# Performance work log

Hardware: AMD Instinct MI355X
Metric: run time of the kernel (lower is better)

## Reference

```python
import jax, jax.numpy as jnp
import numpy as np

CUM_P = 0.9  # cumulative_p
MIN_KEEP = 1  # min_tokens_to_keep (<=1 -> branch is a no-op, as in torch default)


def setup_inputs() -> dict:
    key = jax.random.key(0)
    k1, k2 = jax.random.split(key, 2)
    B, D, V = 64, 2048, 50257
    x = jax.random.normal(k1, (B, D), dtype=jnp.float32)
    W = jax.random.normal(k2, (D, V), dtype=jnp.float32) * (1.0 / np.sqrt(D))
    b = jnp.zeros((V,), dtype=jnp.float32)
    return {"x": x, "W": W, "b": b}


def _nucleus_probs(x, W, b):
    # proj + softmax -> probs over vocab  [B, V]
    probs = jax.nn.softmax(x @ W + b, axis=-1)
    # descending sort over vocab
    sorted_idx = jnp.argsort(-probs, axis=-1)                      # [B, V]
    sorted_p = jnp.take_along_axis(probs, sorted_idx, axis=-1)    # [B, V]
    cum = jnp.cumsum(sorted_p, axis=-1)
    remove_sorted = cum > CUM_P
    # shift right by one so the token that crosses the threshold is kept
    remove_sorted = jnp.concatenate(
        [jnp.zeros_like(remove_sorted[..., :1]), remove_sorted[..., :-1]], axis=-1
    )
    # scatter mask back to original vocab order
    rows = jnp.arange(probs.shape[0])[:, None]                     # [B, 1]
    remove = jnp.zeros_like(remove_sorted).at[rows, sorted_idx].set(remove_sorted)
    kept = jnp.where(remove, 0.0, probs)
    # renormalize exactly as torch: p * 1/(sum + 1e-6)
    return kept * (1.0 / (kept.sum(axis=-1, keepdims=True) + 1e-6))


def reference(x, W, b):
    p = _nucleus_probs(x, W, b)                                    # [B, V]
    # Categorical(probs).sample(); zeros -> log = -inf (never sampled)
    return jax.random.categorical(jax.random.key(42), jnp.log(p), axis=-1)
```

## Files before the change

### kernel.cpp

```cpp
#include <hip/hip_runtime.h>
#include <hip/hip_bf16.h>
#include <stdint.h>

#define BB 64
#define DD 2048
#define VV 50257
#define VP 50260
#define NQ 12565
#define RB 13
#define QPB 967
#define NB 4096
#define MAXC 2048
#define QS 8
#define QCH 6283
#define SK 4

typedef __attribute__((ext_vector_type(8))) short short8;
typedef __attribute__((ext_vector_type(4))) float f32x4;
typedef float f32x4u __attribute__((vector_size(16), aligned(4)));

struct U2 { unsigned x, y; };

__device__ __forceinline__ unsigned rotl32(unsigned v, int r) {
  return (v << r) | (v >> (32 - r));
}

__device__ __forceinline__ U2 threefry2x32(unsigned k0, unsigned k1,
                                           unsigned x0, unsigned x1) {
  unsigned k2 = k0 ^ k1 ^ 0x1BD11BDAu;
  x0 += k0; x1 += k1;
#define TF_R4(r1, r2, r3, r4)                         \
  x0 += x1; x1 = rotl32(x1, r1); x1 ^= x0;            \
  x0 += x1; x1 = rotl32(x1, r2); x1 ^= x0;            \
  x0 += x1; x1 = rotl32(x1, r3); x1 ^= x0;            \
  x0 += x1; x1 = rotl32(x1, r4); x1 ^= x0;
  TF_R4(13, 15, 26, 6)   x0 += k1; x1 += k2 + 1u;
  TF_R4(17, 29, 16, 24)  x0 += k2; x1 += k0 + 2u;
  TF_R4(13, 15, 26, 6)   x0 += k0; x1 += k1 + 3u;
  TF_R4(17, 29, 16, 24)  x0 += k1; x1 += k2 + 4u;
  TF_R4(13, 15, 26, 6)   x0 += k2; x1 += k0 + 5u;
#undef TF_R4
  U2 r; r.x = x0; r.y = x1; return r;
}

__device__ __forceinline__ unsigned jax_random_bits(unsigned e) {
  U2 r = threefry2x32(0u, 42u, 0u, e);
  return r.x ^ r.y;
}

__device__ __forceinline__ unsigned mono_key(float zi) {
  unsigned bb = __float_as_uint(zi);
  return bb ^ ((bb >> 31) ? 0xFFFFFFFFu : 0x80000000u);
}
__device__ __forceinline__ float mono_key_inv(unsigned k) {
  return __uint_as_float((k >> 31) ? (k ^ 0x80000000u) : ~k);
}

__device__ __forceinline__ unsigned short f2bf_hw(float f) {
  __hip_bfloat16 b = __float2bfloat16(f);
  unsigned short u;
  __builtin_memcpy(&u, &b, 2);
  return u;
}
__device__ __forceinline__ float bf2f(unsigned short h) {
  return __uint_as_float(((unsigned)h) << 16);
}

__global__ __launch_bounds__(256) void pack_x_kernel(
    const float* __restrict__ x, unsigned short* __restrict__ xh,
    unsigned short* __restrict__ xl, unsigned* __restrict__ rowmax) {
  if (blockIdx.x == 0 && threadIdx.x < BB) rowmax[threadIdx.x] = 0u;
  int i = blockIdx.x * 256 + threadIdx.x;
  if (i >= 64 * 256) return;
  int b = i >> 8;
  int c = i & 255;
  const float* xp = x + b * 2048 + c * 8;
  short8 hv, lv;
#pragma unroll
  for (int j = 0; j < 8; ++j) {
    float f = xp[j];
    unsigned short h = f2bf_hw(f);
    hv[j] = (short)h;
    lv[j] = (short)f2bf_hw(f - bf2f(h));
  }
  size_t p = ((size_t)c * 64 + b) * 8;
  *(short8*)(xh + p) = hv;
  *(short8*)(xl + p) = lv;
}

__global__ __launch_bounds__(256, 1) void gemm_mfma_kernel(
    const unsigned short* __restrict__ xh, const unsigned short* __restrict__ xl,
    const float* __restrict__ W, float* __restrict__ partial) {
  const int wave = threadIdx.x >> 6;
  const int lane = threadIdx.x & 63;
  const int lo = lane & 15, hi = lane >> 4;
  const int v0w = blockIdx.x * 256 + wave * 64;
  const int vC = v0w + 4 * lo;
  const int ks0 = blockIdx.y * 16;
  const bool edge = (v0w + 64 > VV);

  f32x4 a00 = {0,0,0,0}, a01 = {0,0,0,0}, a02 = {0,0,0,0}, a03 = {0,0,0,0};
  f32x4 a10 = {0,0,0,0}, a11 = {0,0,0,0}, a12 = {0,0,0,0}, a13 = {0,0,0,0};
  f32x4 a20 = {0,0,0,0}, a21 = {0,0,0,0}, a22 = {0,0,0,0}, a23 = {0,0,0,0};
  f32x4 a30 = {0,0,0,0}, a31 = {0,0,0,0}, a32 = {0,0,0,0}, a33 = {0,0,0,0};

  for (int kss = 0; kss < 16; ++kss) {
    const int ks = ks0 + kss;
    const float* wb = W + (size_t)(ks * 32 + hi * 8) * VV;
    f32x4u wq[8];
    if (!edge) {
#pragma unroll
      for (int j = 0; j < 8; ++j)
        wq[j] = *(const f32x4u*)(wb + (size_t)j * VV + vC);
    } else {
#pragma unroll
      for (int j = 0; j < 8; ++j) {
#pragma unroll
        for (int c = 0; c < 4; ++c) {
          int col = vC + c; if (col > VV - 1) col = VV - 1;
          wq[j][c] = wb[(size_t)j * VV + col];
        }
      }
    }
    short8 bh0, bh1, bh2, bh3, bl0, bl1, bl2, bl3;
#pragma unroll
    for (int j = 0; j < 8; ++j) {
      unsigned short h;
      h = f2bf_hw(wq[j][0]); bh0[j] = (short)h; bl0[j] = (short)f2bf_hw(wq[j][0] - bf2f(h));
      h = f2bf_hw(wq[j][1]); bh1[j] = (short)h; bl1[j] = (short)f2bf_hw(wq[j][1] - bf2f(h));
      h = f2bf_hw(wq[j][2]); bh2[j] = (short)h; bl2[j] = (short)f2bf_hw(wq[j][2] - bf2f(h));
      h = f2bf_hw(wq[j][3]); bh3[j] = (short)h; bl3[j] = (short)f2bf_hw(wq[j][3] - bf2f(h));
    }
    const int chunk = ks * 4 + hi;
#define DO_RT(RT, A0, A1, A2, A3)                                           \
    {                                                                       \
      size_t p = ((size_t)chunk * 64 + (RT) * 16 + lo) * 8;                 \
      short8 ah = *(const short8*)(xh + p);                                 \
      short8 al = *(const short8*)(xl + p);                                 \
      A0 = __builtin_amdgcn_mfma_f32_16x16x32_bf16(ah, bh0, A0, 0, 0, 0);   \
      A0 = __builtin_amdgcn_mfma_f32_16x16x32_bf16(al, bh0, A0, 0, 0, 0);   \
      A0 = __builtin_amdgcn_mfma_f32_16x16x32_bf16(ah, bl0, A0, 0, 0, 0);   \
      A1 = __builtin_amdgcn_mfma_f32_16x16x32_bf16(ah, bh1, A1, 0, 0, 0);   \
      A1 = __builtin_amdgcn_mfma_f32_16x16x32_bf16(al, bh1, A1, 0, 0, 0);   \
      A1 = __builtin_amdgcn_mfma_f32_16x16x32_bf16(ah, bl1, A1, 0, 0, 0);   \
      A2 = __builtin_amdgcn_mfma_f32_16x16x32_bf16(ah, bh2, A2, 0, 0, 0);   \
      A2 = __builtin_amdgcn_mfma_f32_16x16x32_bf16(al, bh2, A2, 0, 0, 0);   \
      A2 = __builtin_amdgcn_mfma_f32_16x16x32_bf16(ah, bl2, A2, 0, 0, 0);   \
      A3 = __builtin_amdgcn_mfma_f32_16x16x32_bf16(ah, bh3, A3, 0, 0, 0);   \
      A3 = __builtin_amdgcn_mfma_f32_16x16x32_bf16(al, bh3, A3, 0, 0, 0);   \
      A3 = __builtin_amdgcn_mfma_f32_16x16x32_bf16(ah, bl3, A3, 0, 0, 0);   \
    }
    DO_RT(0, a00, a10, a20, a30)
    DO_RT(1, a01, a11, a21, a31)
    DO_RT(2, a02, a12, a22, a32)
    DO_RT(3, a03, a13, a23, a33)
#undef DO_RT
  }

  float* pp = partial + (size_t)blockIdx.y * BB * VP;
#define ST_RT(RT, A0, A1, A2, A3)                                           \
  {                                                                         \
    _Pragma("unroll")                                                       \
    for (int r = 0; r < 4; ++r) {                                           \
      int row = (RT) * 16 + hi * 4 + r;                                     \
      float4 o; o.x = A0[r]; o.y = A1[r]; o.z = A2[r]; o.w = A3[r];         \
      if (!edge) {                                                          \
        *(float4*)(pp + (size_t)row * VP + vC) = o;                         \
      } else {                                                              \
        if (vC + 0 < VV) pp[(size_t)row * VP + vC + 0] = o.x;               \
        if (vC + 1 < VV) pp[(size_t)row * VP + vC + 1] = o.y;               \
        if (vC + 2 < VV) pp[(size_t)row * VP + vC + 2] = o.z;               \
        if (vC + 3 < VV) pp[(size_t)row * VP + vC + 3] = o.w;               \
      }                                                                     \
    }                                                                       \
  }
  ST_RT(0, a00, a10, a20, a30)
  ST_RT(1, a01, a11, a21, a31)
  ST_RT(2, a02, a12, a22, a32)
  ST_RT(3, a03, a13, a23, a33)
#undef ST_RT
}

__global__ __launch_bounds__(256) void reduce_bias_kernel(
    const float* __restrict__ partial, const float* __restrict__ bias,
    float* __restrict__ logits, unsigned* __restrict__ rowmax) {
  __shared__ float smax[256];
  const int b = blockIdx.y;
  const int q0 = blockIdx.x * QPB;
  const int q1 = (q0 + QPB < NQ) ? q0 + QPB : NQ;
  float mx = -3.4e38f;
  for (int q = q0 + threadIdx.x; q < q1; q += 256) {
    if (q < NQ - 1) {
      int v = q * 4;
      float4 acc = *(const float4*)(bias + v);
#pragma unroll
      for (int s = 0; s < SK; ++s) {
        float4 p = *(const float4*)(partial + ((size_t)s * BB + b) * VP + v);
        acc.x += p.x; acc.y += p.y; acc.z += p.z; acc.w += p.w;
      }
      *(float4*)(logits + (size_t)b * VP + v) = acc;
      mx = fmaxf(mx, fmaxf(fmaxf(acc.x, acc.y), fmaxf(acc.z, acc.w)));
    } else {
      int v = VV - 1;
      float acc = bias[v];
#pragma unroll
      for (int s = 0; s < SK; ++s)
        acc += partial[((size_t)s * BB + b) * VP + v];
      logits[(size_t)b * VP + v] = acc;
      mx = fmaxf(mx, acc);
    }
  }
  smax[threadIdx.x] = mx; __syncthreads();
  for (int s = 128; s > 0; s >>= 1) {
    if (threadIdx.x < s) smax[threadIdx.x] = fmaxf(smax[threadIdx.x], smax[threadIdx.x + s]);
    __syncthreads();
  }
  if (threadIdx.x == 0) atomicMax(rowmax + b, mono_key(smax[0]));
}

__global__ __launch_bounds__(1024) void nucleus_tstar_kernel(
    const float* __restrict__ logits, const unsigned* __restrict__ rowmax,
    unsigned* __restrict__ tstar_out, unsigned long long* __restrict__ pack) {
  __shared__ double sd[1024];
  __shared__ unsigned su[1024];
  __shared__ double bins[NB];
  __shared__ int cidx[MAXC];
  __shared__ unsigned ckey[MAXC];
  __shared__ double cw[MAXC];
  __shared__ int ccount;
  __shared__ int sh_chunk;
  __shared__ int sh_bstar;
  __shared__ double sh_sabove;

  const int row = blockIdx.x;
  const int tid = threadIdx.x;
  const float* z = logits + (size_t)row * VP;
  const float m = mono_key_inv(rowmax[row]);

  for (int i = tid; i < NB; i += 1024) bins[i] = 0.0;
  if (tid == 0) { ccount = 0; sh_chunk = -1; sh_bstar = -1; }
  __syncthreads();

  for (int i = tid; i < VV; i += 1024) {
    float zi = z[i];
    int bin = (int)((m - zi) * 256.0f);
    bin = (bin < 0) ? 0 : ((bin > NB - 1) ? NB - 1 : bin);
    atomicAdd(&bins[bin], (double)expf(zi - m));
  }
  __syncthreads();

  {
    double c = bins[4 * tid] + bins[4 * tid + 1] + bins[4 * tid + 2] + bins[4 * tid + 3];
    sd[tid] = c; __syncthreads();
    for (int off = 1; off < 1024; off <<= 1) {
      double vv = (tid >= off) ? sd[tid - off] : 0.0;
      __syncthreads();
      sd[tid] += vv;
      __syncthreads();
    }
  }
  const double Z = sd[1023];
  const double C = (double)0.9f * Z;

  if (sd[tid] > C && (tid == 0 || sd[tid - 1] <= C)) sh_chunk = tid;
  __syncthreads();
  if (tid == 0) {
    int tc = sh_chunk;
    if (tc >= 0) {
      double run = (tc > 0) ? sd[tc - 1] : 0.0;
      for (int k = 0; k < 4; ++k) {
        double bw = bins[4 * tc + k];
        if (run + bw > C) { sh_bstar = 4 * tc + k; sh_sabove = run; break; }
        run += bw;
      }
    }
  }
  __syncthreads();
  const int bstar = sh_bstar;
  unsigned tkey = 0u;

  if (bstar >= 0) {
    const double Sab = sh_sabove;
    for (int i = tid; i < VV; i += 1024) {
      float zi = z[i];
      int bin = (int)((m - zi) * 256.0f);
      bin = (bin < 0) ? 0 : ((bin > NB - 1) ? NB - 1 : bin);
      if (bin == bstar) {
        int slot = atomicAdd(&ccount, 1);
        if (slot < MAXC) {
          ckey[slot] = mono_key(zi);
          cidx[slot] = i;
          cw[slot] = (double)expf(zi - m);
        }
      }
    }
    __syncthreads();
    int n = ccount; if (n > MAXC) n = MAXC;
    unsigned mk = 0xFFFFFFFFu;
    for (int i = tid; i < n; i += 1024) {
      unsigned ki = ckey[i]; int ii = cidx[i];
      double T = Sab;
      for (int j = 0; j < n; ++j) {
        unsigned kj = ckey[j];
        if (kj > ki || (kj == ki && cidx[j] < ii)) T += cw[j];
      }
      if (T <= C) mk = (ki < mk) ? ki : mk;
    }
    su[tid] = mk; __syncthreads();
    for (int s = 512; s > 0; s >>= 1) {
      if (tid < s) su[tid] = min(su[tid], su[tid + s]);
      __syncthreads();
    }
    tkey = su[0];
  }
  if (tid == 0) { tstar_out[row] = tkey; pack[row] = 0ull; }
}

__global__ __launch_bounds__(1024) void gumbel_kernel(
    const float* __restrict__ logits, const unsigned* __restrict__ tstar_arr,
    unsigned long long* __restrict__ pack) {
  __shared__ float sf[1024];
  __shared__ int si[1024];
  const int row = blockIdx.x >> 3;
  const int q = blockIdx.x & 7;
  const int tid = threadIdx.x;
  const unsigned tstar = tstar_arr[row];
  const float* z = logits + (size_t)row * VP;
  const int i0 = q * QCH;
  const int i1 = (i0 + QCH < VV) ? (i0 + QCH) : VV;

  float best = -3.4e38f; int bidx = 0x7FFFFFFF;
  for (int i = i0 + tid; i < i1; i += 1024) {
    float zi = z[i];
    if (mono_key(zi) < tstar) continue;
    unsigned e = (unsigned)row * (unsigned)VV + (unsigned)i;
    unsigned bits = jax_random_bits(e);
    float f = __uint_as_float((bits >> 9) | 0x3F800000u) - 1.0f;
    float u = fmaxf(1.17549435082228750797e-38f, f);
    float g = -logf(-logf(u));
    float sc = zi + g;
    if (sc > best) { best = sc; bidx = i; }
  }
  sf[tid] = best; si[tid] = bidx; __syncthreads();
  for (int s = 512; s > 0; s >>= 1) {
    if (tid < s) {
      float ob = sf[tid + s]; int oi = si[tid + s];
      if (ob > sf[tid] || (ob == sf[tid] && oi < si[tid])) {
        sf[tid] = ob; si[tid] = oi;
      }
    }
    __syncthreads();
  }
  if (tid == 0 && si[0] != 0x7FFFFFFF) {
    unsigned long long p = ((unsigned long long)mono_key(sf[0]) << 32) |
                           (unsigned long long)(0xFFFFFFFFu - (unsigned)si[0]);
    atomicMax(pack + row, p);
  }
}

__global__ __launch_bounds__(64) void unpack_kernel(
    const unsigned long long* __restrict__ pack, int* __restrict__ out) {
  int r = threadIdx.x;
  if (r < BB) out[r] = (int)(0xFFFFFFFFu - (unsigned)(pack[r] & 0xFFFFFFFFull));
}

extern "C" void kernel_launch(void* const* d_in, const int* in_sizes, int n_in,
                              void* d_out, int out_size, void* d_ws, size_t ws_size,
                              hipStream_t stream) {
  const float* x = (const float*)d_in[0];
  const float* W = (const float*)d_in[1];
  const float* bias = (const float*)d_in[2];
  int* out = (int*)d_out;
  char* ws = (char*)d_ws;

  unsigned short* xh = (unsigned short*)ws;
  unsigned short* xl = (unsigned short*)(ws + 262144);
  float* logits = (float*)(ws + 524288);
  float* partial = (float*)(ws + 13390848);
  unsigned* tstar = (unsigned*)(ws + 64857088);
  unsigned long long* pack = (unsigned long long*)(ws + 64857344);
  unsigned* rowmax = (unsigned*)(ws + 64857856);

  pack_x_kernel<<<64, 256, 0, stream>>>(x, xh, xl, rowmax);
  const int cblocks = (VV + 255) / 256;
  dim3 g(cblocks, SK);
  gemm_mfma_kernel<<<g, 256, 0, stream>>>(xh, xl, W, partial);
  dim3 gr(RB, BB);
  reduce_bias_kernel<<<gr, 256, 0, stream>>>(partial, bias, logits, rowmax);
  nucleus_tstar_kernel<<<BB, 1024, 0, stream>>>(logits, rowmax, tstar, pack);
  gumbel_kernel<<<BB * QS, 1024, 0, stream>>>(logits, tstar, pack);
  unpack_kernel<<<1, 64, 0, stream>>>(pack, out);
}
```

Before: 184.8 us.

## Build histogram in reduce kernel with fixed bin origin, split nucleus into stages

```diff
diff --git a/kernel.cpp b/kernel.cpp
--- a/kernel.cpp
+++ b/kernel.cpp
@@ -9,7 +9,7 @@
 #define NQ 12565
 #define RB 13
 #define QPB 967
-#define NB 4096
+#define HNB 4096
 #define MAXC 2048
 #define QS 8
 #define QCH 6283
@@ -56,6 +56,11 @@
   return __uint_as_float((k >> 31) ? (k ^ 0x80000000u) : ~k);
 }
 
+__device__ __forceinline__ int zbin(float z) {
+  int b = (int)((12.0f - z) * 256.0f);
+  return (b < 0) ? 0 : ((b > HNB - 1) ? HNB - 1 : b);
+}
+
 __device__ __forceinline__ unsigned short f2bf_hw(float f) {
   __hip_bfloat16 b = __float2bfloat16(f);
   unsigned short u;
@@ -68,8 +73,7 @@
 
 __global__ __launch_bounds__(256) void pack_x_kernel(
     const float* __restrict__ x, unsigned short* __restrict__ xh,
-    unsigned short* __restrict__ xl, unsigned* __restrict__ rowmax) {
-  if (blockIdx.x == 0 && threadIdx.x < BB) rowmax[threadIdx.x] = 0u;
+    unsigned short* __restrict__ xl) {
   int i = blockIdx.x * 256 + threadIdx.x;
   if (i >= 64 * 256) return;
   int b = i >> 8;
@@ -183,12 +187,13 @@
 
 __global__ __launch_bounds__(256) void reduce_bias_kernel(
     const float* __restrict__ partial, const float* __restrict__ bias,
-    float* __restrict__ logits, unsigned* __restrict__ rowmax) {
-  __shared__ float smax[256];
+    float* __restrict__ logits, double* __restrict__ hbins) {
+  __shared__ double hb[HNB];
+  for (int i = threadIdx.x; i < HNB; i += 256) hb[i] = 0.0;
+  __syncthreads();
   const int b = blockIdx.y;
   const int q0 = blockIdx.x * QPB;
   const int q1 = (q0 + QPB < NQ) ? q0 + QPB : NQ;
-  float mx = -3.4e38f;
   for (int q = q0 + threadIdx.x; q < q1; q += 256) {
     if (q < NQ - 1) {
       int v = q * 4;
@@ -199,7 +204,10 @@
         acc.x += p.x; acc.y += p.y; acc.z += p.z; acc.w += p.w;
       }
       *(float4*)(logits + (size_t)b * VP + v) = acc;
-      mx = fmaxf(mx, fmaxf(fmaxf(acc.x, acc.y), fmaxf(acc.z, acc.w)));
+      atomicAdd(&hb[zbin(acc.x)], (double)expf(acc.x));
+      atomicAdd(&hb[zbin(acc.y)], (double)expf(acc.y));
+      atomicAdd(&hb[zbin(acc.z)], (double)expf(acc.z));
+      atomicAdd(&hb[zbin(acc.w)], (double)expf(acc.w));
     } else {
       int v = VV - 1;
       float acc = bias[v];
@@ -207,48 +215,32 @@
       for (int s = 0; s < SK; ++s)
         acc += partial[((size_t)s * BB + b) * VP + v];
       logits[(size_t)b * VP + v] = acc;
-      mx = fmaxf(mx, acc);
-    }
-  }
-  smax[threadIdx.x] = mx; __syncthreads();
-  for (int s = 128; s > 0; s >>= 1) {
-    if (threadIdx.x < s) smax[threadIdx.x] = fmaxf(smax[threadIdx.x], smax[threadIdx.x + s]);
-    __syncthreads();
-  }
-  if (threadIdx.x == 0) atomicMax(rowmax + b, mono_key(smax[0]));
-}
-
-__global__ __launch_bounds__(1024) void nucleus_tstar_kernel(
-    const float* __restrict__ logits, const unsigned* __restrict__ rowmax,
-    unsigned* __restrict__ tstar_out, unsigned long long* __restrict__ pack) {
+      atomicAdd(&hb[zbin(acc)], (double)expf(acc));
+    }
+  }
+  __syncthreads();
+  double* outp = hbins + ((size_t)b * RB + blockIdx.x) * HNB;
+  for (int i = threadIdx.x; i < HNB; i += 256) outp[i] = hb[i];
+}
+
+__global__ __launch_bounds__(1024) void bstar_kernel(
+    const double* __restrict__ hbins, int* __restrict__ bstar_out,
+    double* __restrict__ sab_out, double* __restrict__ cval_out,
+    int* __restrict__ gcnt, unsigned long long* __restrict__ pack) {
+  __shared__ double bins[HNB];
   __shared__ double sd[1024];
-  __shared__ unsigned su[1024];
-  __shared__ double bins[NB];
-  __shared__ int cidx[MAXC];
-  __shared__ unsigned ckey[MAXC];
-  __shared__ double cw[MAXC];
-  __shared__ int ccount;
   __shared__ int sh_chunk;
-  __shared__ int sh_bstar;
-  __shared__ double sh_sabove;
-
   const int row = blockIdx.x;
   const int tid = threadIdx.x;
-  const float* z = logits + (size_t)row * VP;
-  const float m = mono_key_inv(rowmax[row]);
-
-  for (int i = tid; i < NB; i += 1024) bins[i] = 0.0;
-  if (tid == 0) { ccount = 0; sh_chunk = -1; sh_bstar = -1; }
+  if (tid == 0) sh_chunk = -1;
+  for (int i = tid; i < HNB; i += 1024) {
+    double s = 0.0;
+    const double* hp = hbins + (size_t)row * RB * HNB + i;
+#pragma unroll
+    for (int p = 0; p < RB; ++p) s += hp[(size_t)p * HNB];
+    bins[i] = s;
+  }
   __syncthreads();
-
-  for (int i = tid; i < VV; i += 1024) {
-    float zi = z[i];
-    int bin = (int)((m - zi) * 256.0f);
-    bin = (bin < 0) ? 0 : ((bin > NB - 1) ? NB - 1 : bin);
-    atomicAdd(&bins[bin], (double)expf(zi - m));
-  }
-  __syncthreads();
-
   {
     double c = bins[4 * tid] + bins[4 * tid + 1] + bins[4 * tid + 2] + bins[4 * tid + 3];
     sd[tid] = c; __syncthreads();
@@ -261,70 +253,34 @@
   }
   const double Z = sd[1023];
   const double C = (double)0.9f * Z;
-
   if (sd[tid] > C && (tid == 0 || sd[tid - 1] <= C)) sh_chunk = tid;
   __syncthreads();
   if (tid == 0) {
     int tc = sh_chunk;
+    int bstar = -1; double sab = 0.0;
     if (tc >= 0) {
       double run = (tc > 0) ? sd[tc - 1] : 0.0;
       for (int k = 0; k < 4; ++k) {
         double bw = bins[4 * tc + k];
-        if (run + bw > C) { sh_bstar = 4 * tc + k; sh_sabove = run; break; }
+        if (run + bw > C) { bstar = 4 * tc + k; sab = run; break; }
         run += bw;
       }
     }
-  }
-  __syncthreads();
-  const int bstar = sh_bstar;
-  unsigned tkey = 0u;
-
-  if (bstar >= 0) {
-    const double Sab = sh_sabove;
-    for (int i = tid; i < VV; i += 1024) {
-      float zi = z[i];
-      int bin = (int)((m - zi) * 256.0f);
-      bin = (bin < 0) ? 0 : ((bin > NB - 1) ? NB - 1 : bin);
-      if (bin == bstar) {
-        int slot = atomicAdd(&ccount, 1);
-        if (slot < MAXC) {
-          ckey[slot] = mono_key(zi);
-          cidx[slot] = i;
-          cw[slot] = (double)expf(zi - m);
-        }
-      }
-    }
-    __syncthreads();
-    int n = ccount; if (n > MAXC) n = MAXC;
-    unsigned mk = 0xFFFFFFFFu;
-    for (int i = tid; i < n; i += 1024) {
-      unsigned ki = ckey[i]; int ii = cidx[i];
-      double T = Sab;
-      for (int j = 0; j < n; ++j) {
-        unsigned kj = ckey[j];
-        if (kj > ki || (kj == ki && cidx[j] < ii)) T += cw[j];
-      }
-      if (T <= C) mk = (ki < mk) ? ki : mk;
-    }
-    su[tid] = mk; __syncthreads();
-    for (int s = 512; s > 0; s >>= 1) {
-      if (tid < s) su[tid] = min(su[tid], su[tid + s]);
-      __syncthreads();
-    }
-    tkey = su[0];
-  }
-  if (tid == 0) { tstar_out[row] = tkey; pack[row] = 0ull; }
-}
-
-__global__ __launch_bounds__(1024) void gumbel_kernel(
-    const float* __restrict__ logits, const unsigned* __restrict__ tstar_arr,
-    unsigned long long* __restrict__ pack) {
+    bstar_out[row] = bstar; sab_out[row] = sab; cval_out[row] = C;
+    gcnt[row] = 0; pack[row] = 0ull;
+  }
+}
+
+__global__ __launch_bounds__(1024) void collect_gumbel_kernel(
+    const float* __restrict__ logits, const int* __restrict__ bstar_arr,
+    int* __restrict__ gcnt, unsigned* __restrict__ gkey, int* __restrict__ gidx,
+    double* __restrict__ gw, unsigned long long* __restrict__ pack) {
   __shared__ float sf[1024];
   __shared__ int si[1024];
   const int row = blockIdx.x >> 3;
   const int q = blockIdx.x & 7;
   const int tid = threadIdx.x;
-  const unsigned tstar = tstar_arr[row];
+  const int bstar = bstar_arr[row];
   const float* z = logits + (size_t)row * VP;
   const int i0 = q * QCH;
   const int i1 = (i0 + QCH < VV) ? (i0 + QCH) : VV;
@@ -332,17 +288,77 @@
   float best = -3.4e38f; int bidx = 0x7FFFFFFF;
   for (int i = i0 + tid; i < i1; i += 1024) {
     float zi = z[i];
-    if (mono_key(zi) < tstar) continue;
-    unsigned e = (unsigned)row * (unsigned)VV + (unsigned)i;
-    unsigned bits = jax_random_bits(e);
-    float f = __uint_as_float((bits >> 9) | 0x3F800000u) - 1.0f;
-    float u = fmaxf(1.17549435082228750797e-38f, f);
-    float g = -logf(-logf(u));
-    float sc = zi + g;
-    if (sc > best) { best = sc; bidx = i; }
+    int bin = zbin(zi);
+    if (bin < bstar) {
+      unsigned e = (unsigned)row * (unsigned)VV + (unsigned)i;
+      unsigned bits = jax_random_bits(e);
+      float f = __uint_as_float((bits >> 9) | 0x3F800000u) - 1.0f;
+      float u = fmaxf(1.17549435082228750797e-38f, f);
+      float g = -logf(-logf(u));
+      float sc = zi + g;
+      if (sc > best || (sc == best && i < bidx)) { best = sc; bidx = i; }
+    } else if (bin == bstar) {
+      int slot = atomicAdd(gcnt + row, 1);
+      if (slot < MAXC) {
+        size_t o = (size_t)row * MAXC + slot;
+        gkey[o] = mono_key(zi);
+        gidx[o] = i;
+        gw[o] = (double)expf(zi);
+      }
+    }
   }
   sf[tid] = best; si[tid] = bidx; __syncthreads();
   for (int s = 512; s > 0; s >>= 1) {
+    if (tid < s) {
+      float ob = sf[tid + s]; int oi = si[tid + s];
+      if (ob > sf[tid] || (ob == sf[tid] && oi < si[tid])) {
+        sf[tid] = ob; si[tid] = oi;
+      }
+    }
+    __syncthreads();
+  }
+  if (tid == 0 && si[0] != 0x7FFFFFFF) {
+    unsigned long long p = ((unsigned long long)mono_key(sf[0]) << 32) |
+                           (unsigned long long)(0xFFFFFFFFu - (unsigned)si[0]);
+    atomicMax(pack + row, p);
+  }
+}
+
+__global__ __launch_bounds__(256) void boundary_kernel(
+    const double* __restrict__ sab_arr, const double* __restrict__ cval_arr,
+    const int* __restrict__ gcnt, const unsigned* __restrict__ gkey,
+    const int* __restrict__ gidx, const double* __restrict__ gw,
+    unsigned long long* __restrict__ pack) {
+  __shared__ float sf[256];
+  __shared__ int si[256];
+  const int row = blockIdx.x;
+  const int tid = threadIdx.x;
+  int n = gcnt[row]; if (n > MAXC) n = MAXC;
+  const double Sab = sab_arr[row];
+  const double C = cval_arr[row];
+  const size_t base = (size_t)row * MAXC;
+
+  float best = -3.4e38f; int bidx = 0x7FFFFFFF;
+  for (int i = tid; i < n; i += 256) {
+    unsigned ki = gkey[base + i]; int ii = gidx[base + i];
+    double T = Sab;
+    for (int j = 0; j < n; ++j) {
+      unsigned kj = gkey[base + j];
+      if (kj > ki || (kj == ki && gidx[base + j] < ii)) T += gw[base + j];
+    }
+    if (T <= C) {
+      float zi = mono_key_inv(ki);
+      unsigned e = (unsigned)row * (unsigned)VV + (unsigned)ii;
+      unsigned bits = jax_random_bits(e);
+      float f = __uint_as_float((bits >> 9) | 0x3F800000u) - 1.0f;
+      float u = fmaxf(1.17549435082228750797e-38f, f);
+      float g = -logf(-logf(u));
+      float sc = zi + g;
+      if (sc > best || (sc == best && ii < bidx)) { best = sc; bidx = ii; }
+    }
+  }
+  sf[tid] = best; si[tid] = bidx; __syncthreads();
+  for (int s = 128; s > 0; s >>= 1) {
     if (tid < s) {
       float ob = sf[tid + s]; int oi = si[tid + s];
       if (ob > sf[tid] || (ob == sf[tid] && oi < si[tid])) {
@@ -377,17 +393,25 @@
   unsigned short* xl = (unsigned short*)(ws + 262144);
   float* logits = (float*)(ws + 524288);
   float* partial = (float*)(ws + 13390848);
-  unsigned* tstar = (unsigned*)(ws + 64857088);
-  unsigned long long* pack = (unsigned long long*)(ws + 64857344);
-  unsigned* rowmax = (unsigned*)(ws + 64857856);
-
-  pack_x_kernel<<<64, 256, 0, stream>>>(x, xh, xl, rowmax);
+  double* hbins = (double*)(ws + 64857088);
+  int* bstar = (int*)(ws + 92120064);
+  double* sab = (double*)(ws + 92120320);
+  double* cval = (double*)(ws + 92120832);
+  int* gcnt = (int*)(ws + 92121344);
+  unsigned long long* pack = (unsigned long long*)(ws + 92121600);
+  unsigned* gkey = (unsigned*)(ws + 92122112);
+  int* gidx = (int*)(ws + 92646400);
+  double* gw = (double*)(ws + 93170688);
+
+  pack_x_kernel<<<64, 256, 0, stream>>>(x, xh, xl);
   const int cblocks = (VV + 255) / 256;
   dim3 g(cblocks, SK);
   gemm_mfma_kernel<<<g, 256, 0, stream>>>(xh, xl, W, partial);
   dim3 gr(RB, BB);
-  reduce_bias_kernel<<<gr, 256, 0, stream>>>(partial, bias, logits, rowmax);
-  nucleus_tstar_kernel<<<BB, 1024, 0, stream>>>(logits, rowmax, tstar, pack);
-  gumbel_kernel<<<BB * QS, 1024, 0, stream>>>(logits, tstar, pack);
+  reduce_bias_kernel<<<gr, 256, 0, stream>>>(partial, bias, logits, hbins);
+  bstar_kernel<<<BB, 1024, 0, stream>>>(hbins, bstar, sab, cval, gcnt, pack);
+  collect_gumbel_kernel<<<BB * QS, 1024, 0, stream>>>(logits, bstar, gcnt,
+                                                      gkey, gidx, gw, pack);
+  boundary_kernel<<<BB, 256, 0, stream>>>(sab, cval, gcnt, gkey, gidx, gw, pack);
   unpack_kernel<<<1, 64, 0, stream>>>(pack, out);
 }
```

After: 186.9 us. No clear change (+1.1%).
